# Kernel tuning notes

Measured on AMD Instinct MI355X. Metric: run time of the kernel, lower is better.

The kernel has to match this reference:

```python
import jax, jax.numpy as jnp
import numpy as np

N_WIRES = 4
N_LAYERS = 2
DIM = 2 ** N_WIRES  # 16
EPS = 1e-5

# PennyLane convention: wire 0 is the most-significant bit of the basis index.
def _bit(i, w):
    return (i >> (N_WIRES - 1 - w)) & 1

# CNOT(control=w, target=(w+1)%N_WIRES) as a basis-state permutation on [DIM]
def _cnot_perm(c, t):
    perm = np.arange(DIM)
    for i in range(DIM):
        if _bit(i, c) == 1:
            perm[i] = i ^ (1 << (N_WIRES - 1 - t))
    return jnp.asarray(perm)

CNOT_PERMS = [_cnot_perm(w, (w + 1) % N_WIRES) for w in range(N_WIRES)]

# PauliZ expectation signs: +1 if bit w of basis state is 0 else -1, shape [N_WIRES, DIM]
SIGNS = jnp.asarray(np.array([[1.0 - 2.0 * _bit(i, w) for i in range(DIM)]
                              for w in range(N_WIRES)], dtype=np.float32))

def _rx(t):
    c = jnp.cos(t / 2).astype(jnp.complex64)
    s = (-1j * jnp.sin(t / 2)).astype(jnp.complex64)
    return jnp.stack([jnp.stack([c, s], -1), jnp.stack([s, c], -1)], -2)

def _ry(t):
    c = jnp.cos(t / 2).astype(jnp.complex64)
    s = jnp.sin(t / 2).astype(jnp.complex64)
    return jnp.stack([jnp.stack([c, -s], -1), jnp.stack([s, c], -1)], -2)

def _rz(t):
    e0 = jnp.exp(-1j * t.astype(jnp.complex64) / 2)
    e1 = jnp.exp(1j * t.astype(jnp.complex64) / 2)
    z = jnp.zeros_like(e0)
    return jnp.stack([jnp.stack([e0, z], -1), jnp.stack([z, e1], -1)], -2)

def _apply1q(state, U, w):
    # state: [B, DIM] complex64; U: [2,2] (shared) or [B,2,2] (per-sample)
    B = state.shape[0]
    st = state.reshape(B, 2 ** w, 2, 2 ** (N_WIRES - 1 - w))
    if U.ndim == 3:
        st = jnp.einsum('blkr,bjk->bljr', st, U)
    else:
        st = jnp.einsum('blkr,jk->bljr', st, U)
    return st.reshape(B, DIM)

def _circuit(angles, weights):
    # angles: [B, N_WIRES] float32, weights: [N_LAYERS, N_WIRES, 3]
    B = angles.shape[0]
    state = jnp.zeros((B, DIM), jnp.complex64).at[:, 0].set(1.0)
    # AngleEmbedding: RX(angle) per wire (per-sample angles)
    for w in range(N_WIRES):
        state = _apply1q(state, _rx(angles[:, w]), w)
    for l in range(N_LAYERS):
        for w in range(N_WIRES):
            state = _apply1q(state, _rx(weights[l, w, 0]), w)
            state = _apply1q(state, _ry(weights[l, w, 1]), w)
            state = _apply1q(state, _rz(weights[l, w, 2]), w)
        for w in range(N_WIRES):
            state = state[:, CNOT_PERMS[w]]
    probs = state.real ** 2 + state.imag ** 2  # [B, DIM]
    return probs @ SIGNS.T  # [B, N_WIRES]

def setup_inputs() -> dict:
    key = jax.random.key(0)
    k1, k2 = jax.random.split(key)
    B = 131072
    x = jax.random.normal(k1, (B, 1, 12, 12), dtype=jnp.float32)
    weights = jax.random.normal(k2, (N_LAYERS, N_WIRES, 3), dtype=jnp.float32)
    gamma = jnp.ones((N_WIRES,), jnp.float32)
    beta = jnp.zeros((N_WIRES,), jnp.float32)
    return {"x": x, "weights": weights, "gamma": gamma, "beta": beta}

def reference(x, weights, gamma, beta):
    B = x.shape[0]
    # avg_pool2d(kernel=6, stride=6) on [B,1,12,12] -> [B,1,2,2] -> [B,4]
    pooled = x.reshape(B, 1, 2, 6, 2, 6).mean(axis=(3, 5)).reshape(B, N_WIRES)
    q = _circuit(pooled, weights)  # [B, 4]
    # dropout p=0 is identity; BatchNorm1d (training mode: batch stats, biased var)
    mean = q.mean(axis=0)
    var = q.var(axis=0)
    return (q - mean) / jnp.sqrt(var + EPS) * gamma + beta
```

## Files before the change

### kernel.cpp

```cpp
#include <hip/hip_runtime.h>

#define WS_SUMS   544
#define N_REP     8

__device__ __forceinline__ constexpr int tri(int i, int j){
  return 16*i - (i*(i-1))/2 + (j - i);
}

__global__ void k_pre(const float* __restrict__ W, float* __restrict__ ws){
  __shared__ float Ur[16][16];
  __shared__ float Uim[16][16];
  const int t = threadIdx.x;

  if (t < N_REP*8) ws[WS_SUMS + t] = 0.f;

  if (t < 16){
    float re[16], im[16];
    #pragma unroll
    for (int i = 0; i < 16; i++){ re[i] = 0.f; im[i] = 0.f; }
    re[t] = 1.f;

    #pragma unroll
    for (int l = 0; l < 2; l++){
      #pragma unroll
      for (int w = 0; w < 4; w++){
        const int m = 8 >> w;
        const float* g = W + (l*4 + w)*3;
        {
          float th = 0.5f*g[0], c = cosf(th), s = sinf(th);
          #pragma unroll
          for (int i0 = 0; i0 < 16; i0++) if (!(i0 & m)){
            int i1 = i0 | m;
            float a0r=re[i0], a0i=im[i0], a1r=re[i1], a1i=im[i1];
            re[i0] = c*a0r + s*a1i;  im[i0] = c*a0i - s*a1r;
            re[i1] = c*a1r + s*a0i;  im[i1] = c*a1i - s*a0r;
          }
        }
        {
          float th = 0.5f*g[1], c = cosf(th), s = sinf(th);
          #pragma unroll
          for (int i0 = 0; i0 < 16; i0++) if (!(i0 & m)){
            int i1 = i0 | m;
            float a0r=re[i0], a0i=im[i0], a1r=re[i1], a1i=im[i1];
            re[i0] = c*a0r - s*a1r;  im[i0] = c*a0i - s*a1i;
            re[i1] = s*a0r + c*a1r;  im[i1] = s*a0i + c*a1i;
          }
        }
        {
          float th = 0.5f*g[2], c = cosf(th), s = sinf(th);
          #pragma unroll
          for (int i0 = 0; i0 < 16; i0++) if (!(i0 & m)){
            int i1 = i0 | m;
            float a0r=re[i0], a0i=im[i0], a1r=re[i1], a1i=im[i1];
            re[i0] = c*a0r + s*a0i;  im[i0] = c*a0i - s*a0r;
            re[i1] = c*a1r - s*a1i;  im[i1] = c*a1i + s*a1r;
          }
        }
      }
      #pragma unroll
      for (int w = 0; w < 4; w++){
        const int mc = 8 >> w, mt = 8 >> ((w+1)&3);
        float nr[16], ni[16];
        #pragma unroll
        for (int i = 0; i < 16; i++){
          int src = (i & mc) ? (i ^ mt) : i;
          nr[i] = re[src]; ni[i] = im[src];
        }
        #pragma unroll
        for (int i = 0; i < 16; i++){ re[i] = nr[i]; im[i] = ni[i]; }
      }
    }
    #pragma unroll
    for (int k = 0; k < 16; k++){ Ur[k][t] = re[k]; Uim[k][t] = im[k]; }
  }
  __syncthreads();

  {
    const int i = t >> 4, j = t & 15;
    if (i <= j){
      const int d = (__popc(i) - __popc(j)) & 3;
      const int n = tri(i, j);
      #pragma unroll
      for (int w = 0; w < 4; w++){
        const int zm = 8 >> w;
        float mr = 0.f, mi = 0.f;
        #pragma unroll
        for (int k = 0; k < 16; k++){
          float z = (k & zm) ? -1.f : 1.f;
          float uir = Ur[k][i], uii = Uim[k][i];
          float ujr = Ur[k][j], uji = Uim[k][j];
          mr += z*(uir*ujr + uii*uji);
          mi += z*(uir*uji - uii*ujr);
        }
        float v = (d == 0) ? mr : (d == 1) ? -mi : (d == 2) ? -mr : mi;
        if (i != j) v *= 2.f;
        ws[n*4 + w] = v;
      }
    }
  }
}

__global__ __launch_bounds__(256) void k_main(const float* __restrict__ x,
                                              const float* __restrict__ A,
                                              float* __restrict__ qout,
                                              float* __restrict__ sums){
  __shared__ float wred[4][8];
  const int t = threadIdx.x;
  const size_t row = (size_t)blockIdx.x*256 + t;
  const float4* rp = (const float4*)(x + row*144);

  float aTL = 0.f, aTR = 0.f, aBL = 0.f, aBR = 0.f;
  #pragma unroll
  for (int ph = 0; ph < 3; ph++){
    float4 buf[12];
    #pragma unroll
    for (int j = 0; j < 12; j++) buf[j] = rp[ph*12 + j];
    #pragma unroll
    for (int j = 0; j < 12; j++){
      const int p  = ph*12 + j;
      const int cg = p % 3;
      float s01 = buf[j].x + buf[j].y, s23 = buf[j].z + buf[j].w;
      float L = (cg == 0) ? (s01 + s23) : ((cg == 1) ? s01 : 0.f);
      float R = (cg == 2) ? (s01 + s23) : ((cg == 1) ? s23 : 0.f);
      if (p < 18){ aTL += L; aTR += R; } else { aBL += L; aBR += R; }
    }
  }

  const float inv = 1.f/72.f;
  float s0,c0,s1,c1,s2,c2,s3,c3;
  __sincosf(aTL*inv, &s0, &c0);
  __sincosf(aTR*inv, &s1, &c1);
  __sincosf(aBL*inv, &s2, &c2);
  __sincosf(aBR*inv, &s3, &c3);

  float t00=c0*c1, t01=c0*s1, t10=s0*c1, t11=s0*s1;
  float u00=c2*c3, u01=c2*s3, u10=s2*c3, u11=s2*s3;
  float r[16];
  r[ 0]=t00*u00; r[ 1]=t00*u01; r[ 2]=t00*u10; r[ 3]=t00*u11;
  r[ 4]=t01*u00; r[ 5]=t01*u01; r[ 6]=t01*u10; r[ 7]=t01*u11;
  r[ 8]=t10*u00; r[ 9]=t10*u01; r[10]=t10*u10; r[11]=t10*u11;
  r[12]=t11*u00; r[13]=t11*u01; r[14]=t11*u10; r[15]=t11*u11;

  float q0=0.f, q1=0.f, q2=0.f, q3=0.f;
  #pragma unroll
  for (int i = 0; i < 16; i++){
    #pragma unroll
    for (int j = i; j < 16; j++){
      const int n = tri(i, j);
      float pij = r[i]*r[j];
      q0 = fmaf(A[n*4+0], pij, q0);
      q1 = fmaf(A[n*4+1], pij, q1);
      q2 = fmaf(A[n*4+2], pij, q2);
      q3 = fmaf(A[n*4+3], pij, q3);
    }
  }

  ((float4*)qout)[row] = make_float4(q0, q1, q2, q3);

  float red[8] = {q0, q1, q2, q3, q0*q0, q1*q1, q2*q2, q3*q3};
  #pragma unroll
  for (int off = 32; off >= 1; off >>= 1){
    #pragma unroll
    for (int k = 0; k < 8; k++) red[k] += __shfl_down(red[k], off, 64);
  }
  const int lane = t & 63, wv = t >> 6;
  if (lane == 0){
    #pragma unroll
    for (int k = 0; k < 8; k++) wred[wv][k] = red[k];
  }
  __syncthreads();
  if (t < 8){
    float s = wred[0][t] + wred[1][t] + wred[2][t] + wred[3][t];
    atomicAdd(&sums[(blockIdx.x & (N_REP-1))*8 + t], s);
  }
}

__global__ __launch_bounds__(256) void k_statsnorm(float* __restrict__ out,
                                                   const float* __restrict__ sums,
                                                   const float* __restrict__ gamma,
                                                   const float* __restrict__ beta,
                                                   float invB){
  const int idx = blockIdx.x*256 + threadIdx.x;
  float sc[4], sh[4];
  #pragma unroll
  for (int w = 0; w < 4; w++){
    float s1 = 0.f, s2 = 0.f;
    #pragma unroll
    for (int rep = 0; rep < N_REP; rep++){
      s1 += sums[rep*8 + w];
      s2 += sums[rep*8 + 4 + w];
    }
    float mean  = s1 * invB;
    float var   = s2 * invB - mean*mean;
    float scale = gamma[w] * rsqrtf(var + 1e-5f);
    sc[w] = scale;
    sh[w] = fmaf(-mean, scale, beta[w]);
  }
  float4* o4 = (float4*)out;
  float4 qv = o4[idx];
  qv.x = fmaf(qv.x, sc[0], sh[0]);
  qv.y = fmaf(qv.y, sc[1], sh[1]);
  qv.z = fmaf(qv.z, sc[2], sh[2]);
  qv.w = fmaf(qv.w, sc[3], sh[3]);
  o4[idx] = qv;
}

extern "C" void kernel_launch(void* const* d_in, const int* in_sizes, int n_in,
                              void* d_out, int out_size, void* d_ws, size_t ws_size,
                              hipStream_t stream){
  const float* x     = (const float*)d_in[0];
  const float* W     = (const float*)d_in[1];
  const float* gamma = (const float*)d_in[2];
  const float* beta  = (const float*)d_in[3];
  float* ws  = (float*)d_ws;
  float* out = (float*)d_out;
  const int B = in_sizes[0] / 144;

  k_pre<<<1, 256, 0, stream>>>(W, ws);
  k_main<<<B/256, 256, 0, stream>>>(x, ws, out, ws + WS_SUMS);
  k_statsnorm<<<B/256, 256, 0, stream>>>(out, ws + WS_SUMS, gamma, beta, 1.f/(float)B);
}
```

Baseline: 127.9 us.

## Rewrite circuit observable in Pauli basis to shrink per-sample quadratic form

Instead of forming the 16-entry state amplitude vector and evaluating a 136-term quadratic form per sample, the precompute kernel expands each observable into the 81-term Pauli (I,Y,Z) product basis for the RX-embedded input state. Each sample then forms products of per-wire factors (1, -sin, cos of the full angle) and contracts with 81 coefficients. This reduces FMAs and constant loads in the main kernel at the cost of a more complex precompute kernel with an extra shared-memory pass.

```diff
diff --git a/kernel.cpp b/kernel.cpp
--- a/kernel.cpp
+++ b/kernel.cpp
@@ -1,15 +1,13 @@
 #include <hip/hip_runtime.h>
 
-#define WS_SUMS   544
+#define WS_SUMS   352
 #define N_REP     8
-
-__device__ __forceinline__ constexpr int tri(int i, int j){
-  return 16*i - (i*(i-1))/2 + (j - i);
-}
 
 __global__ void k_pre(const float* __restrict__ W, float* __restrict__ ws){
   __shared__ float Ur[16][16];
   __shared__ float Uim[16][16];
+  __shared__ float Mr[4][16][16];
+  __shared__ float Mi[4][16][16];
   const int t = threadIdx.x;
 
   if (t < N_REP*8) ws[WS_SUMS + t] = 0.f;
@@ -76,32 +74,54 @@
   __syncthreads();
 
   {
-    const int i = t >> 4, j = t & 15;
-    if (i <= j){
-      const int d = (__popc(i) - __popc(j)) & 3;
-      const int n = tri(i, j);
+    const int j = t >> 4, i = t & 15;
+    #pragma unroll
+    for (int w = 0; w < 4; w++){
+      const int zm = 8 >> w;
+      float mr = 0.f, mi = 0.f;
       #pragma unroll
-      for (int w = 0; w < 4; w++){
-        const int zm = 8 >> w;
-        float mr = 0.f, mi = 0.f;
-        #pragma unroll
-        for (int k = 0; k < 16; k++){
-          float z = (k & zm) ? -1.f : 1.f;
-          float uir = Ur[k][i], uii = Uim[k][i];
-          float ujr = Ur[k][j], uji = Uim[k][j];
-          mr += z*(uir*ujr + uii*uji);
-          mi += z*(uir*uji - uii*ujr);
-        }
-        float v = (d == 0) ? mr : (d == 1) ? -mi : (d == 2) ? -mr : mi;
-        if (i != j) v *= 2.f;
-        ws[n*4 + w] = v;
-      }
+      for (int k = 0; k < 16; k++){
+        float z = (k & zm) ? -1.f : 1.f;
+        float ar = Ur[k][j], ai = Uim[k][j];
+        float br = Ur[k][i], bi = Uim[k][i];
+        mr += z*(ar*br + ai*bi);
+        mi += z*(ar*bi - ai*br);
+      }
+      Mr[w][j][i] = mr;  Mi[w][j][i] = mi;
+    }
+  }
+  __syncthreads();
+
+  if (t < 81){
+    int d0 = t/27, rem = t - d0*27;
+    int d1 = rem/9;  rem -= d1*9;
+    int d2 = rem/3,  d3 = rem - d2*3;
+    int maskY = 0, maskZ = 0, mY = 0;
+    if (d0 == 1){ maskY |= 8; mY++; } else if (d0 == 2) maskZ |= 8;
+    if (d1 == 1){ maskY |= 4; mY++; } else if (d1 == 2) maskZ |= 4;
+    if (d2 == 1){ maskY |= 2; mY++; } else if (d2 == 2) maskZ |= 2;
+    if (d3 == 1){ maskY |= 1; mY++; } else if (d3 == 2) maskZ |= 1;
+    const int mall = maskY | maskZ;
+    const int sel  = mY & 3;
+    #pragma unroll
+    for (int w = 0; w < 4; w++){
+      float c = 0.f;
+      for (int i = 0; i < 16; i++){
+        int j = i ^ maskY;
+        float s = (__popc(i & mall) & 1) ? -1.f : 1.f;
+        float val = (sel == 0) ?  Mr[w][j][i]
+                  : (sel == 1) ?  Mi[w][j][i]
+                  : (sel == 2) ? -Mr[w][j][i]
+                  :              -Mi[w][j][i];
+        c += s * val;
+      }
+      ws[t*4 + w] = c * 0.0625f;
     }
   }
 }
 
 __global__ __launch_bounds__(256) void k_main(const float* __restrict__ x,
-                                              const float* __restrict__ A,
+                                              const float* __restrict__ C,
                                               float* __restrict__ qout,
                                               float* __restrict__ sums){
   __shared__ float wred[4][8];
@@ -126,32 +146,37 @@
     }
   }
 
-  const float inv = 1.f/72.f;
+  const float inv = 1.f/36.f;
   float s0,c0,s1,c1,s2,c2,s3,c3;
   __sincosf(aTL*inv, &s0, &c0);
   __sincosf(aTR*inv, &s1, &c1);
   __sincosf(aBL*inv, &s2, &c2);
   __sincosf(aBR*inv, &s3, &c3);
-
-  float t00=c0*c1, t01=c0*s1, t10=s0*c1, t11=s0*s1;
-  float u00=c2*c3, u01=c2*s3, u10=s2*c3, u11=s2*s3;
-  float r[16];
-  r[ 0]=t00*u00; r[ 1]=t00*u01; r[ 2]=t00*u10; r[ 3]=t00*u11;
-  r[ 4]=t01*u00; r[ 5]=t01*u01; r[ 6]=t01*u10; r[ 7]=t01*u11;
-  r[ 8]=t10*u00; r[ 9]=t10*u01; r[10]=t10*u10; r[11]=t10*u11;
-  r[12]=t11*u00; r[13]=t11*u01; r[14]=t11*u10; r[15]=t11*u11;
+  const float g0[3] = {1.f, -s0, c0};
+  const float g1[3] = {1.f, -s1, c1};
+  const float g2[3] = {1.f, -s2, c2};
+  const float g3[3] = {1.f, -s3, c3};
+
+  float G01[9], G23[9];
+  #pragma unroll
+  for (int a = 0; a < 3; a++)
+    #pragma unroll
+    for (int b = 0; b < 3; b++){
+      G01[a*3+b] = g0[a]*g1[b];
+      G23[a*3+b] = g2[a]*g3[b];
+    }
 
   float q0=0.f, q1=0.f, q2=0.f, q3=0.f;
   #pragma unroll
-  for (int i = 0; i < 16; i++){
-    #pragma unroll
-    for (int j = i; j < 16; j++){
-      const int n = tri(i, j);
-      float pij = r[i]*r[j];
-      q0 = fmaf(A[n*4+0], pij, q0);
-      q1 = fmaf(A[n*4+1], pij, q1);
-      q2 = fmaf(A[n*4+2], pij, q2);
-      q3 = fmaf(A[n*4+3], pij, q3);
+  for (int m = 0; m < 9; m++){
+    #pragma unroll
+    for (int l = 0; l < 9; l++){
+      const int n = m*9 + l;
+      float g = G01[m]*G23[l];
+      q0 = fmaf(C[n*4+0], g, q0);
+      q1 = fmaf(C[n*4+1], g, q1);
+      q2 = fmaf(C[n*4+2], g, q2);
+      q3 = fmaf(C[n*4+3], g, q3);
     }
   }
 
```

Result: slower. 145.2 us (+13.5%).
